# Kernel optimization log

Measured on AMD Instinct MI355X. Metric: run time of the kernel, lower is better.

The kernel has to match this reference:

```python
import jax, jax.numpy as jnp
import numpy as np

N = 100_000      # nodes
E = 1_600_000    # edges (avg degree 16)
F = 64           # node feature dim (node_channels)
H = 64           # hidden_channels
ED = 16          # edge_embedding_size
NEG_SLOPE = 0.2


def _lin(k, fi, fo):
    return jax.random.normal(k, (fi, fo), jnp.float32) / np.sqrt(fi)


def setup_inputs() -> dict:
    key = jax.random.key(0)
    ks = jax.random.split(key, 24)
    inp = {
        "x": jax.random.normal(ks[0], (N, F), jnp.float32),
        "edge_index": jax.random.randint(ks[1], (2, E), 0, N, dtype=jnp.int64),
        "edge_attr": jax.random.normal(ks[2], (E, ED), jnp.float32),
        # conv1 (GATv2Conv -> H)
        "Wl1": _lin(ks[3], F, H), "bl1": jnp.zeros((H,), jnp.float32),
        "Wr1": _lin(ks[4], F, H), "br1": jnp.zeros((H,), jnp.float32),
        "We1": _lin(ks[5], ED, H),
        "a1": jax.random.normal(ks[6], (H,), jnp.float32) / np.sqrt(H),
        "cb1": jnp.zeros((H,), jnp.float32),
        # lin1 residual (F -> H)
        "L1w": _lin(ks[7], F, H), "L1b": jnp.zeros((H,), jnp.float32),
        # conv2 (GATv2Conv -> F)
        "Wl2": _lin(ks[8], H, F), "bl2": jnp.zeros((F,), jnp.float32),
        "Wr2": _lin(ks[9], H, F), "br2": jnp.zeros((F,), jnp.float32),
        "We2": _lin(ks[10], ED, F),
        "a2": jax.random.normal(ks[11], (F,), jnp.float32) / np.sqrt(F),
        "cb2": jnp.zeros((F,), jnp.float32),
        # lin2 residual (H -> F)
        "L2w": _lin(ks[12], H, F), "L2b": jnp.zeros((F,), jnp.float32),
    }
    return inp


def _gatv2(x, src, dst, edge_attr, Wl, bl, Wr, br, We, a, cb):
    # GATv2, heads=1, add_self_loops=False, lin_edge bias-free
    xl = x @ Wl + bl                      # [N, D] source transform (also the value)
    xr = x @ Wr + br                      # [N, D] target transform
    m = xl[src] + xr[dst] + edge_attr @ We  # [E, D]
    s = jax.nn.leaky_relu(m, NEG_SLOPE) @ a  # [E] attention logits
    smax = jax.ops.segment_max(s, dst, num_segments=N)
    ex = jnp.exp(s - smax[dst])
    den = jax.ops.segment_sum(ex, dst, num_segments=N)
    alpha = ex / (den[dst] + 1e-16)       # softmax over incoming edges per target
    out = jax.ops.segment_sum(alpha[:, None] * xl[src], dst, num_segments=N)
    return out + cb


def reference(x, edge_index, edge_attr,
              Wl1, bl1, Wr1, br1, We1, a1, cb1, L1w, L1b,
              Wl2, bl2, Wr2, br2, We2, a2, cb2, L2w, L2b):
    src, dst = edge_index[0], edge_index[1]
    h = _gatv2(x, src, dst, edge_attr, Wl1, bl1, Wr1, br1, We1, a1, cb1) + x @ L1w + L1b
    h = jax.nn.relu(h)
    out = _gatv2(h, src, dst, edge_attr, Wl2, bl2, Wr2, br2, We2, a2, cb2) + h @ L2w + L2b
    return out
```

## Files before the change

### kernel.cpp

```cpp
#include <hip/hip_runtime.h>
#include <hip/hip_fp16.h>
#include <math.h>

#define D 64
#define EDIM 16
#define NEG 0.2f
#define SCHUNK 1024
#define PAD 4

typedef _Float16 hh2 __attribute__((ext_vector_type(2)));
typedef unsigned u32x4 __attribute__((ext_vector_type(4)));
union H2cvt { unsigned u; hh2 v; __half2 h; };

#define DPP_XOR1 0xB1
#define DPP_XOR2 0x4E
#define DPP_XOR3 0x1B
template<int CTRL>
__device__ __forceinline__ float dppx(float v)
{
    return __int_as_float(__builtin_amdgcn_mov_dpp(__float_as_int(v), CTRL, 0xF, 0xF, true));
}

__global__ void node_transform(const float* __restrict__ x,
                               const float* __restrict__ Wl, const float* __restrict__ bl,
                               const float* __restrict__ Wr, const float* __restrict__ br,
                               const float* __restrict__ Lw, const float* __restrict__ Lb,
                               __half* __restrict__ xlh, float* __restrict__ xr,
                               float* __restrict__ res, int N)
{
    __shared__ float wl[D * D], wr[D * D], lw[D * D];
    for (int i = threadIdx.x; i < D * D / 4; i += blockDim.x) {
        ((float4*)wl)[i] = ((const float4*)Wl)[i];
        ((float4*)wr)[i] = ((const float4*)Wr)[i];
        ((float4*)lw)[i] = ((const float4*)Lw)[i];
    }
    int lane = threadIdx.x & 63;
    int wave = __builtin_amdgcn_readfirstlane(threadIdx.x >> 6);
    float vbl = bl[lane], vbr = br[lane], vlb = Lb[lane];
    __syncthreads();

    int gwave  = blockIdx.x * 4 + wave;
    int nwaves = gridDim.x * 4;
    for (int n0 = gwave * 8; n0 < N; n0 += nwaves * 8) {
        float al[8], ar[8], ae[8];
        #pragma unroll
        for (int j = 0; j < 8; j++) { al[j] = vbl; ar[j] = vbr; ae[j] = vlb; }

        if (n0 + 8 <= N) {
            const float* xp0 = x + (size_t)n0 * D;
            #pragma unroll 4
            for (int k = 0; k < D; k++) {
                float w1 = wl[k * D + lane];
                float w2 = wr[k * D + lane];
                float w3 = lw[k * D + lane];
                #pragma unroll
                for (int j = 0; j < 8; j++) {
                    float xv = xp0[j * D + k];
                    al[j] = fmaf(xv, w1, al[j]);
                    ar[j] = fmaf(xv, w2, ar[j]);
                    ae[j] = fmaf(xv, w3, ae[j]);
                }
            }
            #pragma unroll
            for (int j = 0; j < 8; j++) {
                int n = n0 + j;
                xlh[(size_t)n * D + lane] = __float2half(al[j]);
                xr[(size_t)n * D + lane]  = ar[j];
                res[(size_t)n * D + lane] = ae[j];
            }
        } else {
            int nr = N - n0;
            for (int k = 0; k < D; k++) {
                float w1 = wl[k * D + lane];
                float w2 = wr[k * D + lane];
                float w3 = lw[k * D + lane];
                for (int j = 0; j < nr; j++) {
                    float xv = x[(size_t)(n0 + j) * D + k];
                    al[j] = fmaf(xv, w1, al[j]);
                    ar[j] = fmaf(xv, w2, ar[j]);
                    ae[j] = fmaf(xv, w3, ae[j]);
                }
            }
            for (int j = 0; j < nr; j++) {
                int n = n0 + j;
                xlh[(size_t)n * D + lane] = __float2half(al[j]);
                xr[(size_t)n * D + lane]  = ar[j];
                res[(size_t)n * D + lane] = ae[j];
            }
        }
    }
}

__global__ void count_deg(const int* __restrict__ ei, int* __restrict__ degp,
                          int* __restrict__ rank, int E)
{
    int e = blockIdx.x * blockDim.x + threadIdx.x;
    if (e < E) rank[e] = atomicAdd(&degp[ei[E + e] << PAD], 1);
}

__global__ void scan_blocks(const int* __restrict__ degp, int* __restrict__ rowptr,
                            int* __restrict__ bsum, int N)
{
    __shared__ int tsum[256];
    int t = threadIdx.x;
    int base = blockIdx.x * SCHUNK + t * 4;
    int v0 = 0, v1 = 0, v2 = 0, v3 = 0;
    if (base + 0 < N) v0 = degp[(base + 0) << PAD];
    if (base + 1 < N) v1 = degp[(base + 1) << PAD];
    if (base + 2 < N) v2 = degp[(base + 2) << PAD];
    if (base + 3 < N) v3 = degp[(base + 3) << PAD];
    int local = v0 + v1 + v2 + v3;
    tsum[t] = local;
    __syncthreads();
    for (int off = 1; off < 256; off <<= 1) {
        int x = (t >= off) ? tsum[t - off] : 0;
        __syncthreads();
        tsum[t] += x;
        __syncthreads();
    }
    int excl = tsum[t] - local;
    if (base + 0 < N) rowptr[base + 0] = excl;
    if (base + 1 < N) rowptr[base + 1] = excl + v0;
    if (base + 2 < N) rowptr[base + 2] = excl + v0 + v1;
    if (base + 3 < N) rowptr[base + 3] = excl + v0 + v1 + v2;
    if (t == 0) bsum[blockIdx.x] = tsum[255];
}

__global__ void scan_bsums(int* __restrict__ bsum, int nb, int* __restrict__ rowptrN)
{
    __shared__ int part[256];
    int t = threadIdx.x;
    int C = (nb + 255) / 256;
    int b = t * C, e = min(b + C, nb);
    int sum = 0;
    for (int i = b; i < e; i++) sum += bsum[i];
    part[t] = sum;
    __syncthreads();
    for (int off = 1; off < 256; off <<= 1) {
        int x = (t >= off) ? part[t - off] : 0;
        __syncthreads();
        part[t] += x;
        __syncthreads();
    }
    int running = part[t] - sum;
    for (int i = b; i < e; i++) {
        int v = bsum[i];
        bsum[i] = running;
        running += v;
    }
    if (t == 255) *rowptrN = part[255];
}

__global__ void add_offsets(int* __restrict__ rowptr, const int* __restrict__ bsum, int N)
{
    int i = blockIdx.x * blockDim.x + threadIdx.x;
    if (i < N) rowptr[i] += bsum[i >> 10];
}

__global__ void scatter_edges(const int* __restrict__ ei, const float* __restrict__ eattr,
                              const int* __restrict__ rowptr, const int* __restrict__ rank,
                              int* __restrict__ esrc, __half* __restrict__ eah, int E)
{
    int e = blockIdx.x * blockDim.x + threadIdx.x;
    if (e >= E) return;
    int dst = ei[E + e];
    int pos = rowptr[dst] + rank[e];
    esrc[pos] = ei[e];
    const float4* s4 = (const float4*)(eattr + (size_t)e * EDIM);
    float4 f0 = s4[0], f1 = s4[1], f2 = s4[2], f3 = s4[3];
    H2cvt c;
    unsigned w[8];
    c.h = __floats2half2_rn(f0.x, f0.y); w[0] = c.u;
    c.h = __floats2half2_rn(f0.z, f0.w); w[1] = c.u;
    c.h = __floats2half2_rn(f1.x, f1.y); w[2] = c.u;
    c.h = __floats2half2_rn(f1.z, f1.w); w[3] = c.u;
    c.h = __floats2half2_rn(f2.x, f2.y); w[4] = c.u;
    c.h = __floats2half2_rn(f2.z, f2.w); w[5] = c.u;
    c.h = __floats2half2_rn(f3.x, f3.y); w[6] = c.u;
    c.h = __floats2half2_rn(f3.z, f3.w); w[7] = c.u;
    u32x4* d4 = (u32x4*)(eah + (size_t)pos * EDIM);
    d4[0] = (u32x4){w[0], w[1], w[2], w[3]};
    d4[1] = (u32x4){w[4], w[5], w[6], w[7]};
}

__device__ __forceinline__ float bpx(float v, int addr)
{
    return __int_as_float(__builtin_amdgcn_ds_bpermute(addr, __float_as_int(v)));
}

__device__ __forceinline__ float edge_dot(const __half* __restrict__ eah, int ee,
                                          const hh2* w2)
{
    const unsigned* ea = (const unsigned*)(eah + (size_t)ee * EDIM);
    float acc = 0.f;
    #pragma unroll
    for (int k = 0; k < 8; k++) {
        H2cvt c; c.u = ea[k];
#if defined(__has_builtin) && __has_builtin(__builtin_amdgcn_fdot2)
        acc = __builtin_amdgcn_fdot2(c.v, w2[k], acc, false);
#else
        acc += (float)(c.v[0] * w2[k][0]) + (float)(c.v[1] * w2[k][1]);
#endif
    }
    return acc;
}

__global__ void gat_fused(const int* __restrict__ rowptr, const int* __restrict__ esrc,
                          const __half* __restrict__ eah,
                          const float* __restrict__ We, const float* __restrict__ avec,
                          const __half* __restrict__ xlh, const float* __restrict__ xr,
                          const float* __restrict__ res, const float* __restrict__ cb,
                          float* __restrict__ out, int N, int do_relu)
{
    int wid = __builtin_amdgcn_readfirstlane(
        (int)((blockIdx.x * blockDim.x + threadIdx.x) >> 6));
    int lane = threadIdx.x & 63;
    if (wid >= N) return;

    hh2 w2[8];
    #pragma unroll
    for (int j = 0; j < 8; j++) {
        H2cvt c;
        c.h = __floats2half2_rn(We[(2 * j) * D + lane], We[(2 * j + 1) * D + lane]);
        w2[j] = c.v;
    }
    float av  = avec[lane];
    float xrv = xr[(size_t)wid * D + lane];
    int beg = __builtin_amdgcn_readfirstlane(rowptr[wid]);
    int end = __builtin_amdgcn_readfirstlane(rowptr[wid + 1]);

    const int la4 = lane << 2;
    const int A4 = la4 ^ 16, A8 = la4 ^ 32, A16 = la4 ^ 64, A32 = la4 ^ 128;
    int c0 = lane & 1, c1 = lane & 2;

    float S4 = 0.f, Sr = 0.f, O = 0.f;
    int e = beg;
    for (; e + 8 <= end; e += 8) {
        float pA[4], xA[4], pB[4], xB[4];
        #pragma unroll
        for (int j = 0; j < 4; j++) {
            int s = __builtin_amdgcn_readfirstlane(esrc[e + j]);
            xA[j] = __half2float(xlh[(size_t)s * D + lane]);
            float ew = edge_dot(eah, e + j, w2);
            float m = xA[j] + xrv + ew;
            pA[j] = fmaf(NEG, fminf(m, 0.f), fmaxf(m, 0.f)) * av;
        }
        #pragma unroll
        for (int j = 0; j < 4; j++) {
            int s = __builtin_amdgcn_readfirstlane(esrc[e + 4 + j]);
            xB[j] = __half2float(xlh[(size_t)s * D + lane]);
            float ew = edge_dot(eah, e + 4 + j, w2);
            float m = xB[j] + xrv + ew;
            pB[j] = fmaf(NEG, fminf(m, 0.f), fmaxf(m, 0.f)) * av;
        }
        #pragma unroll
        for (int j = 0; j < 4; j++) { pA[j] += dppx<DPP_XOR1>(pA[j]); pB[j] += dppx<DPP_XOR1>(pB[j]); }
        #pragma unroll
        for (int j = 0; j < 4; j++) { pA[j] += dppx<DPP_XOR2>(pA[j]); pB[j] += dppx<DPP_XOR2>(pB[j]); }
        float vA = c1 ? (c0 ? pA[3] : pA[2]) : (c0 ? pA[1] : pA[0]);
        float vB = c1 ? (c0 ? pB[3] : pB[2]) : (c0 ? pB[1] : pB[0]);
        vA += bpx(vA, A4);  vB += bpx(vB, A4);
        vA += bpx(vA, A8);  vB += bpx(vB, A8);
        vA += bpx(vA, A16); vB += bpx(vB, A16);
        vA += bpx(vA, A32); vB += bpx(vB, A32);
        float evA = __expf(vA), evB = __expf(vB);
        S4 += evA; S4 += evB;
        float qA1 = dppx<DPP_XOR1>(evA), qB1 = dppx<DPP_XOR1>(evB);
        float qA2 = dppx<DPP_XOR2>(evA), qB2 = dppx<DPP_XOR2>(evB);
        float qA3 = dppx<DPP_XOR3>(evA), qB3 = dppx<DPP_XOR3>(evB);
        float y0a = c0 ? xA[1] : xA[0], y0b = c0 ? xA[3] : xA[2];
        float y1a = c0 ? xA[0] : xA[1], y1b = c0 ? xA[2] : xA[3];
        float xcA  = c1 ? y0b : y0a, xc1A = c1 ? y1b : y1a;
        float xc2A = c1 ? y0a : y0b, xc3A = c1 ? y1a : y1b;
        O = fmaf(evA, xcA, fmaf(qA1, xc1A, fmaf(qA2, xc2A, fmaf(qA3, xc3A, O))));
        float z0a = c0 ? xB[1] : xB[0], z0b = c0 ? xB[3] : xB[2];
        float z1a = c0 ? xB[0] : xB[1], z1b = c0 ? xB[2] : xB[3];
        float xcB  = c1 ? z0b : z0a, xc1B = c1 ? z1b : z1a;
        float xc2B = c1 ? z0a : z0b, xc3B = c1 ? z1a : z1b;
        O = fmaf(evB, xcB, fmaf(qB1, xc1B, fmaf(qB2, xc2B, fmaf(qB3, xc3B, O))));
    }
    for (; e + 4 <= end; e += 4) {
        float pp[4], xlv[4];
        #pragma unroll
        for (int j = 0; j < 4; j++) {
            int s = __builtin_amdgcn_readfirstlane(esrc[e + j]);
            xlv[j] = __half2float(xlh[(size_t)s * D + lane]);
            float ew = edge_dot(eah, e + j, w2);
            float m = xlv[j] + xrv + ew;
            pp[j] = fmaf(NEG, fminf(m, 0.f), fmaxf(m, 0.f)) * av;
        }
        #pragma unroll
        for (int j = 0; j < 4; j++) pp[j] += dppx<DPP_XOR1>(pp[j]);
        #pragma unroll
        for (int j = 0; j < 4; j++) pp[j] += dppx<DPP_XOR2>(pp[j]);
        float t0 = c0 ? pp[1] : pp[0];
        float t1 = c0 ? pp[3] : pp[2];
        float v  = c1 ? t1 : t0;
        v += bpx(v, A4); v += bpx(v, A8); v += bpx(v, A16); v += bpx(v, A32);
        float ev = __expf(v);
        S4 += ev;
        float q1 = dppx<DPP_XOR1>(ev);
        float q2 = dppx<DPP_XOR2>(ev);
        float q3 = dppx<DPP_XOR3>(ev);
        float y0a = c0 ? xlv[1] : xlv[0], y0b = c0 ? xlv[3] : xlv[2];
        float y1a = c0 ? xlv[0] : xlv[1], y1b = c0 ? xlv[2] : xlv[3];
        float x_c  = c1 ? y0b : y0a;
        float x_c1 = c1 ? y1b : y1a;
        float x_c2 = c1 ? y0a : y0b;
        float x_c3 = c1 ? y1a : y1b;
        O = fmaf(ev, x_c, fmaf(q1, x_c1, fmaf(q2, x_c2, fmaf(q3, x_c3, O))));
    }
    for (; e < end; ++e) {
        int s = __builtin_amdgcn_readfirstlane(esrc[e]);
        float xlv = __half2float(xlh[(size_t)s * D + lane]);
        float ew = edge_dot(eah, e, w2);
        float m = xlv + xrv + ew;
        float p = fmaf(NEG, fminf(m, 0.f), fmaxf(m, 0.f)) * av;
        p += dppx<DPP_XOR1>(p); p += dppx<DPP_XOR2>(p);
        p += bpx(p, A4); p += bpx(p, A8); p += bpx(p, A16); p += bpx(p, A32);
        float w = __expf(p);
        Sr += w;
        O = fmaf(w, xlv, O);
    }
    S4 += dppx<DPP_XOR1>(S4);
    S4 += dppx<DPP_XOR2>(S4);
    float S = S4 + Sr;

    float v = O / (S + 1e-16f) + cb[lane] + res[(size_t)wid * D + lane];
    if (do_relu) v = fmaxf(v, 0.f);
    out[(size_t)wid * D + lane] = v;
}

extern "C" void kernel_launch(void* const* d_in, const int* in_sizes, int n_in,
                              void* d_out, int out_size, void* d_ws, size_t ws_size,
                              hipStream_t stream)
{
    const float* x     = (const float*)d_in[0];
    const int*   ei    = (const int*)d_in[1];
    const float* eattr = (const float*)d_in[2];
    const float* Wl1 = (const float*)d_in[3];  const float* bl1 = (const float*)d_in[4];
    const float* Wr1 = (const float*)d_in[5];  const float* br1 = (const float*)d_in[6];
    const float* We1 = (const float*)d_in[7];  const float* a1  = (const float*)d_in[8];
    const float* cb1 = (const float*)d_in[9];
    const float* L1w = (const float*)d_in[10]; const float* L1b = (const float*)d_in[11];
    const float* Wl2 = (const float*)d_in[12]; const float* bl2 = (const float*)d_in[13];
    const float* Wr2 = (const float*)d_in[14]; const float* br2 = (const float*)d_in[15];
    const float* We2 = (const float*)d_in[16]; const float* a2  = (const float*)d_in[17];
    const float* cb2 = (const float*)d_in[18];
    const float* L2w = (const float*)d_in[19]; const float* L2b = (const float*)d_in[20];

    const int N = in_sizes[0] / D;
    const int E = in_sizes[1] / 2;
    const int NB = (N + SCHUNK - 1) / SCHUNK;

    char* wsb = (char*)d_ws;
    float*  xr   = (float*)wsb;  wsb += (size_t)N * D * sizeof(float);
    float*  res  = (float*)wsb;  wsb += (size_t)N * D * sizeof(float);
    __half* xlh  = (__half*)wsb; wsb += (size_t)N * D * sizeof(__half);
    __half* eah  = (__half*)wsb; wsb += (size_t)E * EDIM * sizeof(__half);
    int* esrc    = (int*)wsb;    wsb += (size_t)E * sizeof(int);
    int* rowptr  = (int*)wsb;    wsb += (size_t)(N + 1) * sizeof(int);
    int* bsum    = (int*)wsb;    wsb += (size_t)NB * sizeof(int);
    int* degp    = (int*)res;
    int* rank    = (int*)xlh;

    float* out = (float*)d_out;

    const int et = (E + 255) / 256;
    const int nb = (N + 3) / 4;

    hipMemsetAsync(degp, 0, ((size_t)N << PAD) * sizeof(int), stream);
    count_deg<<<et, 256, 0, stream>>>(ei, degp, rank, E);
    scan_blocks<<<NB, 256, 0, stream>>>(degp, rowptr, bsum, N);
    scan_bsums<<<1, 256, 0, stream>>>(bsum, NB, rowptr + N);
    add_offsets<<<(N + 255) / 256, 256, 0, stream>>>(rowptr, bsum, N);
    scatter_edges<<<et, 256, 0, stream>>>(ei, eattr, rowptr, rank, esrc, eah, E);

    node_transform<<<1024, 256, 0, stream>>>(x, Wl1, bl1, Wr1, br1, L1w, L1b,
                                             xlh, xr, res, N);
    gat_fused<<<nb, 256, 0, stream>>>(rowptr, esrc, eah, We1, a1,
                                      xlh, xr, res, cb1, out, N, 1);

    node_transform<<<1024, 256, 0, stream>>>(out, Wl2, bl2, Wr2, br2, L2w, L2b,
                                             xlh, xr, res, N);
    gat_fused<<<nb, 256, 0, stream>>>(rowptr, esrc, eah, We2, a2,
                                      xlh, xr, res, cb2, out, N, 0);
}
```

Measured before the change: 476.2 us.

## Double-buffer edge loads in GAT aggregation and mask tail edges

Restructures the per-node edge loop into 4-edge packets. The source index, half-precision edge attributes and gathered xl value for the next packet are prefetched into registers while the current packet is computed, which aims to hide gather latency. The 8-edge unroll and the scalar remainder loop are replaced by one loop: out-of-range tail edges are clamped to a valid index and their logits are forced to a large negative value so they contribute nothing. Zero-degree nodes now exit early. In exchange, register use rises with the doubled buffers, and less independent work sits in each iteration than in the old 8-edge body.

```diff
diff --git a/kernel.cpp b/kernel.cpp
--- a/kernel.cpp
+++ b/kernel.cpp
@@ -7,6 +7,7 @@
 #define NEG 0.2f
 #define SCHUNK 1024
 #define PAD 4
+#define NEGINF -1e30f
 
 typedef _Float16 hh2 __attribute__((ext_vector_type(2)));
 typedef unsigned u32x4 __attribute__((ext_vector_type(4)));
@@ -188,10 +189,8 @@
     return __int_as_float(__builtin_amdgcn_ds_bpermute(addr, __float_as_int(v)));
 }
 
-__device__ __forceinline__ float edge_dot(const __half* __restrict__ eah, int ee,
-                                          const hh2* w2)
-{
-    const unsigned* ea = (const unsigned*)(eah + (size_t)ee * EDIM);
+__device__ __forceinline__ float edge_dot_w(const unsigned* ea, const hh2* w2)
+{
     float acc = 0.f;
     #pragma unroll
     for (int k = 0; k < 8; k++) {
@@ -217,6 +216,18 @@
     int lane = threadIdx.x & 63;
     if (wid >= N) return;
 
+    int beg = __builtin_amdgcn_readfirstlane(rowptr[wid]);
+    int end = __builtin_amdgcn_readfirstlane(rowptr[wid + 1]);
+    int nE  = end - beg;
+
+    float base_add = cb[lane] + res[(size_t)wid * D + lane];
+    if (nE == 0) {
+        float v = base_add;
+        if (do_relu) v = fmaxf(v, 0.f);
+        out[(size_t)wid * D + lane] = v;
+        return;
+    }
+
     hh2 w2[8];
     #pragma unroll
     for (int j = 0; j < 8; j++) {
@@ -226,69 +237,57 @@
     }
     float av  = avec[lane];
     float xrv = xr[(size_t)wid * D + lane];
-    int beg = __builtin_amdgcn_readfirstlane(rowptr[wid]);
-    int end = __builtin_amdgcn_readfirstlane(rowptr[wid + 1]);
 
     const int la4 = lane << 2;
     const int A4 = la4 ^ 16, A8 = la4 ^ 32, A16 = la4 ^ 64, A32 = la4 ^ 128;
     int c0 = lane & 1, c1 = lane & 2;
 
-    float S4 = 0.f, Sr = 0.f, O = 0.f;
-    int e = beg;
-    for (; e + 8 <= end; e += 8) {
-        float pA[4], xA[4], pB[4], xB[4];
+    int npk = (nE + 3) >> 2;
+
+    int  sC[4];      unsigned eaC[4][8];  float xC[4];
+    int  sN[4];      unsigned eaN[4][8];  float xN[4];
+
+    #pragma unroll
+    for (int j = 0; j < 4; j++) {
+        int idx = beg + j; if (idx > end - 1) idx = end - 1;
+        idx = __builtin_amdgcn_readfirstlane(idx);
+        sC[j] = __builtin_amdgcn_readfirstlane(esrc[idx]);
+        const unsigned* ea = (const unsigned*)(eah + (size_t)idx * EDIM);
+        #pragma unroll
+        for (int k = 0; k < 8; k++) eaC[j][k] = ea[k];
+    }
+    #pragma unroll
+    for (int j = 0; j < 4; j++)
+        xC[j] = __half2float(xlh[(size_t)sC[j] * D + lane]);
+
+    float S4 = 0.f, O = 0.f;
+    for (int p = 0; p < npk; ++p) {
+        if (p + 1 < npk) {
+            int b1 = beg + ((p + 1) << 2);
+            #pragma unroll
+            for (int j = 0; j < 4; j++) {
+                int idx = b1 + j; if (idx > end - 1) idx = end - 1;
+                idx = __builtin_amdgcn_readfirstlane(idx);
+                sN[j] = __builtin_amdgcn_readfirstlane(esrc[idx]);
+                const unsigned* ea = (const unsigned*)(eah + (size_t)idx * EDIM);
+                #pragma unroll
+                for (int k = 0; k < 8; k++) eaN[j][k] = ea[k];
+            }
+            #pragma unroll
+            for (int j = 0; j < 4; j++)
+                xN[j] = __half2float(xlh[(size_t)sN[j] * D + lane]);
+        }
+        int rem = nE - (p << 2);
+        float pp[4];
         #pragma unroll
         for (int j = 0; j < 4; j++) {
-            int s = __builtin_amdgcn_readfirstlane(esrc[e + j]);
-            xA[j] = __half2float(xlh[(size_t)s * D + lane]);
-            float ew = edge_dot(eah, e + j, w2);
-            float m = xA[j] + xrv + ew;
-            pA[j] = fmaf(NEG, fminf(m, 0.f), fmaxf(m, 0.f)) * av;
-        }
-        #pragma unroll
-        for (int j = 0; j < 4; j++) {
-            int s = __builtin_amdgcn_readfirstlane(esrc[e + 4 + j]);
-            xB[j] = __half2float(xlh[(size_t)s * D + lane]);
-            float ew = edge_dot(eah, e + 4 + j, w2);
-            float m = xB[j] + xrv + ew;
-            pB[j] = fmaf(NEG, fminf(m, 0.f), fmaxf(m, 0.f)) * av;
-        }
-        #pragma unroll
-        for (int j = 0; j < 4; j++) { pA[j] += dppx<DPP_XOR1>(pA[j]); pB[j] += dppx<DPP_XOR1>(pB[j]); }
-        #pragma unroll
-        for (int j = 0; j < 4; j++) { pA[j] += dppx<DPP_XOR2>(pA[j]); pB[j] += dppx<DPP_XOR2>(pB[j]); }
-        float vA = c1 ? (c0 ? pA[3] : pA[2]) : (c0 ? pA[1] : pA[0]);
-        float vB = c1 ? (c0 ? pB[3] : pB[2]) : (c0 ? pB[1] : pB[0]);
-        vA += bpx(vA, A4);  vB += bpx(vB, A4);
-        vA += bpx(vA, A8);  vB += bpx(vB, A8);
-        vA += bpx(vA, A16); vB += bpx(vB, A16);
-        vA += bpx(vA, A32); vB += bpx(vB, A32);
-        float evA = __expf(vA), evB = __expf(vB);
-        S4 += evA; S4 += evB;
-        float qA1 = dppx<DPP_XOR1>(evA), qB1 = dppx<DPP_XOR1>(evB);
-        float qA2 = dppx<DPP_XOR2>(evA), qB2 = dppx<DPP_XOR2>(evB);
-        float qA3 = dppx<DPP_XOR3>(evA), qB3 = dppx<DPP_XOR3>(evB);
-        float y0a = c0 ? xA[1] : xA[0], y0b = c0 ? xA[3] : xA[2];
-        float y1a = c0 ? xA[0] : xA[1], y1b = c0 ? xA[2] : xA[3];
-        float xcA  = c1 ? y0b : y0a, xc1A = c1 ? y1b : y1a;
-        float xc2A = c1 ? y0a : y0b, xc3A = c1 ? y1a : y1b;
-        O = fmaf(evA, xcA, fmaf(qA1, xc1A, fmaf(qA2, xc2A, fmaf(qA3, xc3A, O))));
-        float z0a = c0 ? xB[1] : xB[0], z0b = c0 ? xB[3] : xB[2];
-        float z1a = c0 ? xB[0] : xB[1], z1b = c0 ? xB[2] : xB[3];
-        float xcB  = c1 ? z0b : z0a, xc1B = c1 ? z1b : z1a;
-        float xc2B = c1 ? z0a : z0b, xc3B = c1 ? z1a : z1b;
-        O = fmaf(evB, xcB, fmaf(qB1, xc1B, fmaf(qB2, xc2B, fmaf(qB3, xc3B, O))));
-    }
-    for (; e + 4 <= end; e += 4) {
-        float pp[4], xlv[4];
-        #pragma unroll
-        for (int j = 0; j < 4; j++) {
-            int s = __builtin_amdgcn_readfirstlane(esrc[e + j]);
-            xlv[j] = __half2float(xlh[(size_t)s * D + lane]);
-            float ew = edge_dot(eah, e + j, w2);
-            float m = xlv[j] + xrv + ew;
+            float ew = edge_dot_w(eaC[j], w2);
+            float m = xC[j] + xrv + ew;
             pp[j] = fmaf(NEG, fminf(m, 0.f), fmaxf(m, 0.f)) * av;
         }
+        if (rem < 2) pp[1] = NEGINF;
+        if (rem < 3) pp[2] = NEGINF;
+        if (rem < 4) pp[3] = NEGINF;
         #pragma unroll
         for (int j = 0; j < 4; j++) pp[j] += dppx<DPP_XOR1>(pp[j]);
         #pragma unroll
@@ -302,31 +301,27 @@
         float q1 = dppx<DPP_XOR1>(ev);
         float q2 = dppx<DPP_XOR2>(ev);
         float q3 = dppx<DPP_XOR3>(ev);
-        float y0a = c0 ? xlv[1] : xlv[0], y0b = c0 ? xlv[3] : xlv[2];
-        float y1a = c0 ? xlv[0] : xlv[1], y1b = c0 ? xlv[2] : xlv[3];
+        float y0a = c0 ? xC[1] : xC[0], y0b = c0 ? xC[3] : xC[2];
+        float y1a = c0 ? xC[0] : xC[1], y1b = c0 ? xC[2] : xC[3];
         float x_c  = c1 ? y0b : y0a;
         float x_c1 = c1 ? y1b : y1a;
         float x_c2 = c1 ? y0a : y0b;
         float x_c3 = c1 ? y1a : y1b;
         O = fmaf(ev, x_c, fmaf(q1, x_c1, fmaf(q2, x_c2, fmaf(q3, x_c3, O))));
-    }
-    for (; e < end; ++e) {
-        int s = __builtin_amdgcn_readfirstlane(esrc[e]);
-        float xlv = __half2float(xlh[(size_t)s * D + lane]);
-        float ew = edge_dot(eah, e, w2);
-        float m = xlv + xrv + ew;
-        float p = fmaf(NEG, fminf(m, 0.f), fmaxf(m, 0.f)) * av;
-        p += dppx<DPP_XOR1>(p); p += dppx<DPP_XOR2>(p);
-        p += bpx(p, A4); p += bpx(p, A8); p += bpx(p, A16); p += bpx(p, A32);
-        float w = __expf(p);
-        Sr += w;
-        O = fmaf(w, xlv, O);
+        if (p + 1 < npk) {
+            #pragma unroll
+            for (int j = 0; j < 4; j++) {
+                sC[j] = sN[j];
+                xC[j] = xN[j];
+                #pragma unroll
+                for (int k = 0; k < 8; k++) eaC[j][k] = eaN[j][k];
+            }
+        }
     }
     S4 += dppx<DPP_XOR1>(S4);
     S4 += dppx<DPP_XOR2>(S4);
-    float S = S4 + Sr;
-
-    float v = O / (S + 1e-16f) + cb[lane] + res[(size_t)wid * D + lane];
+
+    float v = O / (S4 + 1e-16f) + base_add;
     if (do_relu) v = fmaxf(v, 0.f);
     out[(size_t)wid * D + lane] = v;
 }
```

Result: slower. 513.2 us (+7.8%).
